# Performance work log

Measured on AMD Instinct MI355X. Metric: run time of the kernel, lower is better.

Reference implementation:

```python
import jax, jax.numpy as jnp
import numpy as np

DIM = 192
R = 16            # patches_resolution, D=H=W=R
SP = 4            # split_size
NH = 6            # num_heads (block level); per-branch heads = NH//3
B = 2
L = R * R * R
EPS = 1e-5


def layernorm(x, g, b):
    mu = jnp.mean(x, axis=-1, keepdims=True)
    var = jnp.mean(jnp.square(x - mu), axis=-1, keepdims=True)
    return (x - mu) * jax.lax.rsqrt(var + EPS) * g + b


def window_partition(x, d_sp, h_sp, w_sp, nh):
    b, _, _, _, cb = x.shape
    win = d_sp * h_sp * w_sp
    x = x.reshape(b, R // d_sp, d_sp, R // h_sp, h_sp, R // w_sp, w_sp, cb)
    x = x.transpose(0, 1, 3, 5, 2, 4, 6, 7).reshape(-1, win, nh, cb // nh)
    return x.transpose(0, 2, 1, 3)


def window_merge(x, d_sp, h_sp, w_sp, b):
    cb = x.shape[-1]
    x = x.reshape(b, R // d_sp, R // h_sp, R // w_sp, d_sp, h_sp, w_sp, cb)
    x = x.transpose(0, 1, 4, 2, 5, 3, 6, 7).reshape(b, L, cb)
    return x


def lepe_attention(q, k, v, d_sp, h_sp, w_sp, nh):
    # q,k,v: (B, L, Cb). Note: LePE bias is computed-but-unused in the source -> pure windowed SDPA.
    b, _, cb = q.shape
    hd = cb // nh
    scale = hd ** -0.5
    q5 = q.reshape(b, R, R, R, cb)
    k5 = k.reshape(b, R, R, R, cb)
    v5 = v.reshape(b, R, R, R, cb)
    qw = window_partition(q5, d_sp, h_sp, w_sp, nh) * scale
    kw = window_partition(k5, d_sp, h_sp, w_sp, nh)
    vw = window_partition(v5, d_sp, h_sp, w_sp, nh)
    attn = jax.nn.softmax(jnp.einsum('whqd,whkd->whqk', qw, kw), axis=-1)
    out = jnp.einsum('whqk,whkd->whqd', attn, vw)
    out = out.transpose(0, 2, 1, 3).reshape(-1, d_sp * h_sp * w_sp, cb)
    return window_merge(out, d_sp, h_sp, w_sp, b)


WINDOW_SHAPES = [(R, R, SP), (R, SP, R), (SP, R, R)]  # idx 0,1,2


def setup_inputs() -> dict:
    key = jax.random.key(0)
    ks = jax.random.split(key, 12)
    C = DIM
    H4 = int(C * 4)
    inp = {
        'x': jax.random.normal(ks[0], (B, C, R, R, R), dtype=jnp.float32),
        'w_qkv': jax.random.normal(ks[1], (C, 3 * C), dtype=jnp.float32) * (C ** -0.5),
        'w_proj': jax.random.normal(ks[2], (C, C), dtype=jnp.float32) * (C ** -0.5),
        'b_proj': jnp.zeros((C,), dtype=jnp.float32),
        'g1': jnp.ones((C,), dtype=jnp.float32),
        'b1': jnp.zeros((C,), dtype=jnp.float32),
        'g2': jnp.ones((C,), dtype=jnp.float32),
        'b2': jnp.zeros((C,), dtype=jnp.float32),
        'w_fc1': jax.random.normal(ks[3], (C, H4), dtype=jnp.float32) * (C ** -0.5),
        'b_fc1': jnp.zeros((H4,), dtype=jnp.float32),
        'w_fc2': jax.random.normal(ks[4], (H4, C), dtype=jnp.float32) * (H4 ** -0.5),
        'b_fc2': jnp.zeros((C,), dtype=jnp.float32),
    }
    return inp


def reference(x, w_qkv, w_proj, b_proj, g1, b1, g2, b2, w_fc1, b_fc1, w_fc2, b_fc2):
    C = DIM
    Cb = C // 3
    nh_b = NH // 3
    x = 2.0 * x
    xt = jnp.transpose(x, (0, 2, 3, 4, 1))                # (B, D, H, W, C)
    img = layernorm(xt, g1, b1)
    qkv = img.reshape(B, L, C) @ w_qkv                    # (B, L, 3C)
    q, k, v = jnp.split(qkv.reshape(B, L, 3, C).transpose(2, 0, 1, 3), 3, axis=0)
    q, k, v = q[0], k[0], v[0]                            # each (B, L, C)
    outs = []
    for i, (dsp, hsp, wsp) in enumerate(WINDOW_SHAPES):
        sl = slice(i * Cb, (i + 1) * Cb)
        outs.append(lepe_attention(q[..., sl], k[..., sl], v[..., sl], dsp, hsp, wsp, nh_b))
    attened = jnp.concatenate(outs, axis=2)               # (B, L, C)
    attened = attened @ w_proj + b_proj
    xs = xt.reshape(B, L, C) + attened
    h = layernorm(xs, g2, b2) @ w_fc1 + b_fc1
    h = jax.nn.gelu(h, approximate=False)
    xs = xs + (h @ w_fc2 + b_fc2)
    out = xs.reshape(B, R, R, R, C).transpose(0, 4, 1, 2, 3)  # (B, C, D, H, W)
    return out
```

## Files before the change

### kernel.cpp

```cpp
#include <hip/hip_runtime.h>
#include <hip/hip_bf16.h>

typedef __hip_bfloat16 bf16;
typedef short short8 __attribute__((ext_vector_type(8)));
typedef float floatx4 __attribute__((ext_vector_type(4)));

#define SZ (8192*192)

__device__ __forceinline__ unsigned short f2b(float f) {
    unsigned u = __builtin_bit_cast(unsigned, f);
    u += 0x7FFFu + ((u >> 16) & 1u);
    return (unsigned short)(u >> 16);
}
__device__ __forceinline__ float b2f(unsigned short h) {
    unsigned u = ((unsigned)h) << 16;
    return __builtin_bit_cast(float, u);
}
__device__ __forceinline__ unsigned pk2(float a, float b) {
    return ((unsigned)f2b(b) << 16) | (unsigned)f2b(a);
}

__global__ void detect_kernel(const unsigned short* __restrict__ x16, int* __restrict__ flag) {
    __shared__ int cnt;
    if (threadIdx.x == 0) cnt = 0;
    __syncthreads();
    int c = 0;
    for (int i = threadIdx.x; i < 8192; i += 256) {
        int e = (x16[i] >> 7) & 0xFF;
        if (e >= 152) c++;
    }
    if (c) atomicAdd(&cnt, c);
    __syncthreads();
    if (threadIdx.x == 0) *flag = (cnt >= 32) ? 1 : 0;
}

struct WPA { const void* s[11]; };

__global__ __launch_bounds__(256) void wprep_kernel(WPA a, unsigned short* __restrict__ wdst,
                                                    float* __restrict__ vdst,
                                                    const int* __restrict__ flag) {
    int i = blockIdx.x * 256 + threadIdx.x;
    int f = *flag;
    if (i < 442368) {
        int seg, base, K, N;
        if (i < 110592)      { seg = 0; base = 0;      K = 192; N = 576; }
        else if (i < 147456) { seg = 1; base = 110592; K = 192; N = 192; }
        else if (i < 294912) { seg = 2; base = 147456; K = 192; N = 768; }
        else                 { seg = 3; base = 294912; K = 768; N = 192; }
        int j = i - base;
        int n = j / K, k = j - n * K;
        size_t src = (size_t)k * N + n;
        float v = f ? ((const float*)a.s[seg])[src] : b2f(((const unsigned short*)a.s[seg])[src]);
        wdst[i] = f2b(v);
    } else if (i < 444288) {
        int j = i - 442368;
        int seg, off;
        if (j < 960)       { seg = 4 + j / 192; off = j % 192; }
        else if (j < 1728) { seg = 9; off = j - 960; }
        else               { seg = 10; off = j - 1728; }
        float v = f ? ((const float*)a.s[seg])[off] : b2f(((const unsigned short*)a.s[seg])[off]);
        vdst[j] = v;
    }
}

__global__ __launch_bounds__(256) void prep_kernel(const void* __restrict__ xin,
        const int* __restrict__ flag,
        const float* __restrict__ g1, const float* __restrict__ b1,
        float* __restrict__ xt, unsigned short* __restrict__ img) {
    __shared__ float tile[192][33];
    __shared__ float mu[32], rs[32];
    int tid = threadIdx.x;
    int t0 = blockIdx.x * 32;
    int b = t0 >> 12;
    int ts = t0 & 4095;
    int f = *flag;
    for (int idx = tid; idx < 192 * 32; idx += 256) {
        int c = idx >> 5, tt = idx & 31;
        int gi = ((b * 192 + c) << 12) + ts + tt;
        float raw = f ? ((const float*)xin)[gi] : b2f(((const unsigned short*)xin)[gi]);
        tile[c][tt] = 2.0f * raw;
    }
    __syncthreads();
    if (tid < 32) {
        float s = 0.f, sq = 0.f;
        for (int c = 0; c < 192; ++c) { float v = tile[c][tid]; s += v; sq += v * v; }
        float m = s * (1.0f / 192.0f);
        float var = sq * (1.0f / 192.0f) - m * m;
        mu[tid] = m;
        rs[tid] = rsqrtf(var + 1e-5f);
    }
    __syncthreads();
    for (int idx = tid; idx < 32 * 192; idx += 256) {
        int tt = idx / 192, c = idx % 192;
        float v = tile[c][tt];
        int o = (t0 + tt) * 192 + c;
        xt[o] = v;
        img[o] = f2b((v - mu[tt]) * rs[tt] * g1[c] + b1[c]);
    }
}

template <int MODE>
__global__ __launch_bounds__(256) void mfma_gemm(const unsigned short* __restrict__ A,
        const unsigned short* __restrict__ WT, const float* __restrict__ bias,
        const float* __restrict__ resid, void* __restrict__ out, int M, int N, int K) {
    int wave = threadIdx.x >> 6, lane = threadIdx.x & 63;
    int quad = lane >> 4, l16 = lane & 15;
    int m0 = blockIdx.x * 128, n0 = blockIdx.y * 64;
    const unsigned short* ap = A + (size_t)(m0 + wave * 32 + l16) * K + quad * 8;
    const unsigned short* wp = WT + (size_t)(n0 + l16) * K + quad * 8;
    floatx4 acc[2][4] = {};
    #pragma unroll 2
    for (int kc = 0; kc < K; kc += 32) {
        short8 a0 = *reinterpret_cast<const short8*>(ap + kc);
        short8 a1 = *reinterpret_cast<const short8*>(ap + (size_t)16 * K + kc);
        #pragma unroll
        for (int nt = 0; nt < 4; ++nt) {
            short8 w = *reinterpret_cast<const short8*>(wp + (size_t)nt * 16 * K + kc);
            acc[0][nt] = __builtin_amdgcn_mfma_f32_16x16x32_bf16(a0, w, acc[0][nt], 0, 0, 0);
            acc[1][nt] = __builtin_amdgcn_mfma_f32_16x16x32_bf16(a1, w, acc[1][nt], 0, 0, 0);
        }
    }
    #pragma unroll
    for (int fh = 0; fh < 2; ++fh) {
        #pragma unroll
        for (int nt = 0; nt < 4; ++nt) {
            #pragma unroll
            for (int r = 0; r < 4; ++r) {
                int row = m0 + wave * 32 + fh * 16 + quad * 4 + r;
                int col = n0 + nt * 16 + l16;
                float v = acc[fh][nt][r];
                if (MODE == 0 && col < 192) v *= 0.17677669529663689f;
                if (MODE >= 1) v += bias[col];
                if (MODE == 2) v = 0.5f * v * (1.0f + erff(v * 0.70710678118654752f));
                size_t o = (size_t)row * N + col;
                if (MODE == 0 || MODE == 2) ((unsigned short*)out)[o] = f2b(v);
                else                        ((float*)out)[o] = v + resid[o];
            }
        }
    }
}

__device__ __forceinline__ int tok_of(int br, int wb, int q) {
    if (br == 0) return ((q >> 6) << 8) | (((q >> 2) & 15) << 4) | (wb << 2) | (q & 3);
    else if (br == 1) return ((q >> 6) << 8) | (((wb << 2) + ((q >> 4) & 3)) << 4) | (q & 15);
    else return (((wb << 2) + (q >> 8)) << 8) | (q & 255);
}

__device__ __forceinline__ int vtaddr(int d) { return d * 72 + ((d >> 3) << 3); }

__device__ __forceinline__ const short8* kvptr(const unsigned short* __restrict__ qkv,
                                               int tb, int br, int wb, int q, int off) {
    int t = tok_of(br, wb, q);
    return reinterpret_cast<const short8*>(qkv + (size_t)(tb + t) * 576 + off);
}

template <int SPLIT>
__global__ __launch_bounds__(256) void attn_mfma(const unsigned short* __restrict__ qkv,
        unsigned short* __restrict__ attb, float* __restrict__ po, float* __restrict__ pl) {
    __shared__ __align__(16) unsigned short P[4][16 * 72];
    __shared__ __align__(16) unsigned short VT[2][32 * 72 + 32];
    const int chunk = 96 * SPLIT;
    int hw = blockIdx.x;
    int bid = (hw & 7) * chunk + (hw >> 3);
    int kh, rest;
    if (SPLIT == 2) { kh = bid & 1; rest = bid >> 1; }
    else            { kh = 0;       rest = bid; }
    int qt = rest & 15, head = (rest >> 4) & 1, wb = (rest >> 5) & 3, b = (rest >> 7) & 1, br = rest >> 8;
    int tid = threadIdx.x;
    int wave = tid >> 6, lane = tid & 63, quad = lane >> 4, l16 = lane & 15;
    int coff = br * 64 + head * 32;
    int tb = b << 12;
    int tq = tok_of(br, wb, qt * 64 + wave * 16 + l16);
    short8 aq = *reinterpret_cast<const short8*>(qkv + (size_t)(tb + tq) * 576 + coff + quad * 8);
    floatx4 o0 = {}, o1 = {};
    float lsum[4] = {0.f, 0.f, 0.f, 0.f};
    unsigned short* Pw = P[wave];
    int vkey5 = lane >> 2;
    int vd = lane & 3;
    int vcol = 4 * vkey5 + wave;

    const int NT = 16 / SPLIT;
    const int kt0 = kh * NT;

    short8 vv, k0, k1, k2, k3;
    {
        int kc = kt0 * 64;
        vv = *kvptr(qkv, tb, br, wb, kc + wave * 16 + vkey5, 384 + coff + vd * 8);
        k0 = *kvptr(qkv, tb, br, wb, kc + l16,      192 + coff + quad * 8);
        k1 = *kvptr(qkv, tb, br, wb, kc + 16 + l16, 192 + coff + quad * 8);
        k2 = *kvptr(qkv, tb, br, wb, kc + 32 + l16, 192 + coff + quad * 8);
        k3 = *kvptr(qkv, tb, br, wb, kc + 48 + l16, 192 + coff + quad * 8);
    }

    for (int it = 0; it < NT; ++it) {
        unsigned short* VTb = VT[it & 1];
        #pragma unroll
        for (int j = 0; j < 8; ++j)
            VTb[vtaddr(vd * 8 + j) + vcol] = (unsigned short)vv[j];
        short8 ck0 = k0, ck1 = k1, ck2 = k2, ck3 = k3;
        if (it + 1 < NT) {
            int kc = (kt0 + it + 1) * 64;
            vv = *kvptr(qkv, tb, br, wb, kc + wave * 16 + vkey5, 384 + coff + vd * 8);
            k0 = *kvptr(qkv, tb, br, wb, kc + l16,      192 + coff + quad * 8);
            k1 = *kvptr(qkv, tb, br, wb, kc + 16 + l16, 192 + coff + quad * 8);
            k2 = *kvptr(qkv, tb, br, wb, kc + 32 + l16, 192 + coff + quad * 8);
            k3 = *kvptr(qkv, tb, br, wb, kc + 48 + l16, 192 + coff + quad * 8);
        }
        __syncthreads();
        floatx4 z = {};
        floatx4 s0 = __builtin_amdgcn_mfma_f32_16x16x32_bf16(aq, ck0, z, 0, 0, 0);
        floatx4 s1 = __builtin_amdgcn_mfma_f32_16x16x32_bf16(aq, ck1, z, 0, 0, 0);
        floatx4 s2 = __builtin_amdgcn_mfma_f32_16x16x32_bf16(aq, ck2, z, 0, 0, 0);
        floatx4 s3 = __builtin_amdgcn_mfma_f32_16x16x32_bf16(aq, ck3, z, 0, 0, 0);
        #pragma unroll
        for (int r = 0; r < 4; ++r) {
            float p0 = __expf(s0[r]);
            float p1 = __expf(s1[r]);
            float p2 = __expf(s2[r]);
            float p3 = __expf(s3[r]);
            lsum[r] += (p0 + p1) + (p2 + p3);
            uint2 w2; w2.x = pk2(p0, p1); w2.y = pk2(p2, p3);
            *reinterpret_cast<uint2*>(Pw + (quad * 4 + r) * 72 + 4 * l16) = w2;
        }
        const unsigned short* pr = Pw + l16 * 72;
        short8 a0 = *reinterpret_cast<const short8*>(pr + quad * 8);
        short8 a1 = *reinterpret_cast<const short8*>(pr + 32 + quad * 8);
        const unsigned short* v0r = VTb + vtaddr(l16);
        const unsigned short* v1r = VTb + vtaddr(16 + l16);
        short8 b00 = *reinterpret_cast<const short8*>(v0r + quad * 8);
        short8 b01 = *reinterpret_cast<const short8*>(v0r + 32 + quad * 8);
        short8 b10 = *reinterpret_cast<const short8*>(v1r + quad * 8);
        short8 b11 = *reinterpret_cast<const short8*>(v1r + 32 + quad * 8);
        o0 = __builtin_amdgcn_mfma_f32_16x16x32_bf16(a0, b00, o0, 0, 0, 0);
        o0 = __builtin_amdgcn_mfma_f32_16x16x32_bf16(a1, b01, o0, 0, 0, 0);
        o1 = __builtin_amdgcn_mfma_f32_16x16x32_bf16(a0, b10, o1, 0, 0, 0);
        o1 = __builtin_amdgcn_mfma_f32_16x16x32_bf16(a1, b11, o1, 0, 0, 0);
    }
    #pragma unroll
    for (int r = 0; r < 4; ++r) {
        float ls = lsum[r];
        ls += __shfl_xor(ls, 1);
        ls += __shfl_xor(ls, 2);
        ls += __shfl_xor(ls, 4);
        ls += __shfl_xor(ls, 8);
        lsum[r] = ls;
    }
    if (SPLIT == 2) {
        #pragma unroll
        for (int r = 0; r < 4; ++r) {
            int q = qt * 64 + wave * 16 + quad * 4 + r;
            int t = tok_of(br, wb, q);
            size_t o = ((size_t)(kh << 13) + tb + t) * 192 + coff;
            po[o + l16]      = o0[r];
            po[o + 16 + l16] = o1[r];
            if (l16 == 0) pl[(size_t)((kh << 13) + tb + t) * 6 + br * 2 + head] = lsum[r];
        }
    } else {
        #pragma unroll
        for (int r = 0; r < 4; ++r) {
            float inv = 1.0f / lsum[r];
            int q = qt * 64 + wave * 16 + quad * 4 + r;
            int t = tok_of(br, wb, q);
            size_t o = (size_t)(tb + t) * 192 + coff;
            attb[o + l16]      = f2b(o0[r] * inv);
            attb[o + 16 + l16] = f2b(o1[r] * inv);
        }
    }
}

__global__ __launch_bounds__(256) void attn_combine(const float* __restrict__ po,
        const float* __restrict__ pl, unsigned short* __restrict__ attb) {
    int token = (blockIdx.x << 2) + (threadIdx.x >> 6);
    int lane = threadIdx.x & 63;
    const float* r0 = po + (size_t)token * 192;
    const float* r1 = r0 + (size_t)8192 * 192;
    const float* q0 = pl + (size_t)token * 6;
    const float* q1 = q0 + (size_t)8192 * 6;
    unsigned short* orow = attb + (size_t)token * 192;
    #pragma unroll
    for (int sgm = 0; sgm < 3; ++sgm) {
        int d = lane + sgm * 64;
        int g = d >> 5;
        float denom = q0[g] + q1[g];
        orow[d] = f2b((r0[d] + r1[d]) / denom);
    }
}

__global__ __launch_bounds__(256) void ln_kernel(const float* __restrict__ in,
        const float* __restrict__ g, const float* __restrict__ bb, unsigned short* __restrict__ out) {
    int token = (blockIdx.x << 2) + (threadIdx.x >> 6);
    int lane = threadIdx.x & 63;
    const float* row = in + (size_t)token * 192;
    float v0 = row[lane], v1 = row[lane + 64], v2 = row[lane + 128];
    float s = v0 + v1 + v2, sq = v0 * v0 + v1 * v1 + v2 * v2;
    #pragma unroll
    for (int mask = 1; mask < 64; mask <<= 1) {
        s += __shfl_xor(s, mask);
        sq += __shfl_xor(sq, mask);
    }
    float m = s * (1.f / 192.f);
    float var = sq * (1.f / 192.f) - m * m;
    float rsd = rsqrtf(var + 1e-5f);
    unsigned short* orow = out + (size_t)token * 192;
    orow[lane]       = f2b((v0 - m) * rsd * g[lane]       + bb[lane]);
    orow[lane + 64]  = f2b((v1 - m) * rsd * g[lane + 64]  + bb[lane + 64]);
    orow[lane + 128] = f2b((v2 - m) * rsd * g[lane + 128] + bb[lane + 128]);
}

__global__ __launch_bounds__(256) void unprep_kernel(const float* __restrict__ xs,
                                                     void* __restrict__ out,
                                                     const int* __restrict__ flag) {
    __shared__ float tile[192][33];
    int tid = threadIdx.x;
    int t0 = blockIdx.x * 32;
    int b = t0 >> 12, ts = t0 & 4095;
    for (int idx = tid; idx < 32 * 192; idx += 256) {
        int tt = idx / 192, c = idx % 192;
        tile[c][tt] = xs[(size_t)(t0 + tt) * 192 + c];
    }
    __syncthreads();
    int f = *flag;
    for (int idx = tid; idx < 192 * 32; idx += 256) {
        int c = idx >> 5, tt = idx & 31;
        float v = tile[c][tt];
        int o = ((b * 192 + c) << 12) + ts + tt;
        if (f) ((float*)out)[o] = v;
        else   ((unsigned short*)out)[o] = f2b(v);
    }
}

extern "C" void kernel_launch(void* const* d_in, const int* in_sizes, int n_in,
                              void* d_out, int out_size, void* d_ws, size_t ws_size,
                              hipStream_t stream) {
    float* ws = (float*)d_ws;

    float* vbase = ws;
    float* bprojf = vbase + 0;
    float* g1f    = vbase + 192;
    float* b1f    = vbase + 384;
    float* g2f    = vbase + 576;
    float* b2f    = vbase + 768;
    float* bfc1f  = vbase + 960;
    float* bfc2f  = vbase + 1728;

    unsigned short* wbase = (unsigned short*)(ws + 1920);
    unsigned short* wqkvT = wbase + 0;
    unsigned short* wprojT = wbase + 110592;
    unsigned short* wfc1T = wbase + 147456;
    unsigned short* wfc2T = wbase + 294912;

    size_t p = 1920 + 442368 / 2;
    float* xt = ws + p; p += SZ;
    unsigned short* img = (unsigned short*)(ws + p); p += SZ / 2;
    size_t pQ = p;
    unsigned short* qkv = (unsigned short*)(ws + pQ);
    unsigned short* hbuf = (unsigned short*)(ws + pQ);
    p = pQ + 8192 * 768 / 2;
    unsigned short* attb = (unsigned short*)(ws + p); p += SZ / 2;
    int* flag = (int*)(ws + p); p += 16;
    float* po = ws + p; p += (size_t)2 * 8192 * 192;
    float* pl = ws + p; p += (size_t)2 * 8192 * 6;
    bool split_ok = ws_size >= p * sizeof(float);
    float* xs = xt;
    unsigned short* lnb = img;

    WPA wa;
    wa.s[0] = d_in[1];  wa.s[1] = d_in[2];  wa.s[2] = d_in[8];  wa.s[3] = d_in[10];
    wa.s[4] = d_in[3];  wa.s[5] = d_in[4];  wa.s[6] = d_in[5];  wa.s[7] = d_in[6];
    wa.s[8] = d_in[7];  wa.s[9] = d_in[9];  wa.s[10] = d_in[11];

    detect_kernel<<<dim3(1), dim3(256), 0, stream>>>((const unsigned short*)d_in[0], flag);
    wprep_kernel<<<dim3(1736), dim3(256), 0, stream>>>(wa, wbase, vbase, flag);
    prep_kernel<<<dim3(256), dim3(256), 0, stream>>>(d_in[0], flag, g1f, b1f, xt, img);
    mfma_gemm<0><<<dim3(64, 9), dim3(256), 0, stream>>>(img, wqkvT, nullptr, nullptr, qkv, 8192, 576, 192);
    if (split_ok) {
        attn_mfma<2><<<dim3(1536), dim3(256), 0, stream>>>(qkv, nullptr, po, pl);
        attn_combine<<<dim3(2048), dim3(256), 0, stream>>>(po, pl, attb);
    } else {
        attn_mfma<1><<<dim3(768), dim3(256), 0, stream>>>(qkv, attb, nullptr, nullptr);
    }
    mfma_gemm<1><<<dim3(64, 3), dim3(256), 0, stream>>>(attb, wprojT, bprojf, xt, xs, 8192, 192, 192);
    ln_kernel<<<dim3(2048), dim3(256), 0, stream>>>(xs, g2f, b2f, lnb);
    mfma_gemm<2><<<dim3(64, 12), dim3(256), 0, stream>>>(lnb, wfc1T, bfc1f, nullptr, hbuf, 8192, 768, 192);
    mfma_gemm<3><<<dim3(64, 3), dim3(256), 0, stream>>>(hbuf, wfc2T, bfc2f, xs, xs, 8192, 192, 768);
    unprep_kernel<<<dim3(256), dim3(256), 0, stream>>>(xs, d_out, flag);
}
```

Baseline: 211.9 us.

## Fuse attention combine into proj GEMM and output transpose into FC2 epilogue

Removes the attn_combine kernel by having the projection GEMM read the two fp32 partial attention outputs and log-sum denominators, normalising and converting them to bf16 on the fly as its A operand. Removes unprep_kernel by writing the FC2 result, plus residual, directly in channel-major output layout inside the GEMM epilogue. It also halves the GEMM M tile to 64 rows to launch twice as many blocks. In exchange, the proj GEMM does uncoalesced scalar fp32 loads in its inner loop, and the FC2 epilogue makes strided transposed stores without staging through LDS.

```diff
diff --git a/kernel.cpp b/kernel.cpp
--- a/kernel.cpp
+++ b/kernel.cpp
@@ -99,42 +99,74 @@
     }
 }
 
-template <int MODE>
+template <int MODE, int TM>
 __global__ __launch_bounds__(256) void mfma_gemm(const unsigned short* __restrict__ A,
+        const float* __restrict__ pA, const float* __restrict__ pl,
         const unsigned short* __restrict__ WT, const float* __restrict__ bias,
-        const float* __restrict__ resid, void* __restrict__ out, int M, int N, int K) {
+        const float* __restrict__ resid, void* __restrict__ out,
+        const int* __restrict__ flag, int N, int K) {
     int wave = threadIdx.x >> 6, lane = threadIdx.x & 63;
     int quad = lane >> 4, l16 = lane & 15;
-    int m0 = blockIdx.x * 128, n0 = blockIdx.y * 64;
-    const unsigned short* ap = A + (size_t)(m0 + wave * 32 + l16) * K + quad * 8;
+    int m0 = blockIdx.x * TM, n0 = blockIdx.y * 64;
+    constexpr int FH = TM / 64;
+    int arow = m0 + wave * (TM / 4) + l16;
+    const unsigned short* ap = A + (size_t)arow * K + quad * 8;
     const unsigned short* wp = WT + (size_t)(n0 + l16) * K + quad * 8;
-    floatx4 acc[2][4] = {};
+    floatx4 acc[FH][4] = {};
+    float inv6[6];
+    const float* prow0 = nullptr;
+    if constexpr (MODE == 4) {
+        prow0 = pA + (size_t)arow * 192;
+        #pragma unroll
+        for (int g = 0; g < 6; ++g)
+            inv6[g] = 1.0f / (pl[(size_t)arow * 6 + g] + pl[(size_t)(8192 + arow) * 6 + g]);
+    }
     #pragma unroll 2
     for (int kc = 0; kc < K; kc += 32) {
-        short8 a0 = *reinterpret_cast<const short8*>(ap + kc);
-        short8 a1 = *reinterpret_cast<const short8*>(ap + (size_t)16 * K + kc);
+        short8 a0, a1;
+        if constexpr (MODE == 4) {
+            float iv = inv6[kc >> 5];
+            const float* p0 = prow0 + kc + quad * 8;
+            const float* p1 = p0 + (size_t)8192 * 192;
+            #pragma unroll
+            for (int j = 0; j < 8; ++j) a0[j] = (short)f2b((p0[j] + p1[j]) * iv);
+        } else {
+            a0 = *reinterpret_cast<const short8*>(ap + kc);
+            if constexpr (FH == 2) a1 = *reinterpret_cast<const short8*>(ap + (size_t)16 * K + kc);
+        }
         #pragma unroll
         for (int nt = 0; nt < 4; ++nt) {
             short8 w = *reinterpret_cast<const short8*>(wp + (size_t)nt * 16 * K + kc);
             acc[0][nt] = __builtin_amdgcn_mfma_f32_16x16x32_bf16(a0, w, acc[0][nt], 0, 0, 0);
-            acc[1][nt] = __builtin_amdgcn_mfma_f32_16x16x32_bf16(a1, w, acc[1][nt], 0, 0, 0);
-        }
-    }
+            if constexpr (FH == 2)
+                acc[1][nt] = __builtin_amdgcn_mfma_f32_16x16x32_bf16(a1, w, acc[1][nt], 0, 0, 0);
+        }
+    }
+    int f = 0;
+    if constexpr (MODE == 5) f = *flag;
     #pragma unroll
-    for (int fh = 0; fh < 2; ++fh) {
+    for (int fh = 0; fh < FH; ++fh) {
         #pragma unroll
         for (int nt = 0; nt < 4; ++nt) {
             #pragma unroll
             for (int r = 0; r < 4; ++r) {
-                int row = m0 + wave * 32 + fh * 16 + quad * 4 + r;
+                int row = m0 + wave * (TM / 4) + fh * 16 + quad * 4 + r;
                 int col = n0 + nt * 16 + l16;
                 float v = acc[fh][nt][r];
                 if (MODE == 0 && col < 192) v *= 0.17677669529663689f;
                 if (MODE >= 1) v += bias[col];
                 if (MODE == 2) v = 0.5f * v * (1.0f + erff(v * 0.70710678118654752f));
-                size_t o = (size_t)row * N + col;
-                if (MODE == 0 || MODE == 2) ((unsigned short*)out)[o] = f2b(v);
-                else                        ((float*)out)[o] = v + resid[o];
+                if constexpr (MODE == 5) {
+                    v += resid[(size_t)row * 192 + col];
+                    int bb_ = row >> 12, t = row & 4095;
+                    size_t o = ((size_t)(bb_ * 192 + col) << 12) + t;
+                    if (f) ((float*)out)[o] = v;
+                    else   ((unsigned short*)out)[o] = f2b(v);
+                } else {
+                    size_t o = (size_t)row * N + col;
+                    if (MODE == 0 || MODE == 2) ((unsigned short*)out)[o] = f2b(v);
+                    else                        ((float*)out)[o] = v + resid[o];
+                }
             }
         }
     }
@@ -268,24 +300,6 @@
     }
 }
 
-__global__ __launch_bounds__(256) void attn_combine(const float* __restrict__ po,
-        const float* __restrict__ pl, unsigned short* __restrict__ attb) {
-    int token = (blockIdx.x << 2) + (threadIdx.x >> 6);
-    int lane = threadIdx.x & 63;
-    const float* r0 = po + (size_t)token * 192;
-    const float* r1 = r0 + (size_t)8192 * 192;
-    const float* q0 = pl + (size_t)token * 6;
-    const float* q1 = q0 + (size_t)8192 * 6;
-    unsigned short* orow = attb + (size_t)token * 192;
-    #pragma unroll
-    for (int sgm = 0; sgm < 3; ++sgm) {
-        int d = lane + sgm * 64;
-        int g = d >> 5;
-        float denom = q0[g] + q1[g];
-        orow[d] = f2b((r0[d] + r1[d]) / denom);
-    }
-}
-
 __global__ __launch_bounds__(256) void ln_kernel(const float* __restrict__ in,
         const float* __restrict__ g, const float* __restrict__ bb, unsigned short* __restrict__ out) {
     int token = (blockIdx.x << 2) + (threadIdx.x >> 6);
@@ -305,28 +319,6 @@
     orow[lane]       = f2b((v0 - m) * rsd * g[lane]       + bb[lane]);
     orow[lane + 64]  = f2b((v1 - m) * rsd * g[lane + 64]  + bb[lane + 64]);
     orow[lane + 128] = f2b((v2 - m) * rsd * g[lane + 128] + bb[lane + 128]);
-}
-
-__global__ __launch_bounds__(256) void unprep_kernel(const float* __restrict__ xs,
-                                                     void* __restrict__ out,
-                                                     const int* __restrict__ flag) {
-    __shared__ float tile[192][33];
-    int tid = threadIdx.x;
-    int t0 = blockIdx.x * 32;
-    int b = t0 >> 12, ts = t0 & 4095;
-    for (int idx = tid; idx < 32 * 192; idx += 256) {
-        int tt = idx / 192, c = idx % 192;
-        tile[c][tt] = xs[(size_t)(t0 + tt) * 192 + c];
-    }
-    __syncthreads();
-    int f = *flag;
-    for (int idx = tid; idx < 192 * 32; idx += 256) {
-        int c = idx >> 5, tt = idx & 31;
-        float v = tile[c][tt];
-        int o = ((b * 192 + c) << 12) + ts + tt;
-        if (f) ((float*)out)[o] = v;
-        else   ((unsigned short*)out)[o] = f2b(v);
-    }
 }
 
 extern "C" void kernel_launch(void* const* d_in, const int* in_sizes, int n_in,
@@ -372,16 +364,20 @@
     detect_kernel<<<dim3(1), dim3(256), 0, stream>>>((const unsigned short*)d_in[0], flag);
     wprep_kernel<<<dim3(1736), dim3(256), 0, stream>>>(wa, wbase, vbase, flag);
     prep_kernel<<<dim3(256), dim3(256), 0, stream>>>(d_in[0], flag, g1f, b1f, xt, img);
-    mfma_gemm<0><<<dim3(64, 9), dim3(256), 0, stream>>>(img, wqkvT, nullptr, nullptr, qkv, 8192, 576, 192);
+    mfma_gemm<0, 64><<<dim3(128, 9), dim3(256), 0, stream>>>(
+        img, nullptr, nullptr, wqkvT, nullptr, nullptr, qkv, nullptr, 576, 192);
     if (split_ok) {
         attn_mfma<2><<<dim3(1536), dim3(256), 0, stream>>>(qkv, nullptr, po, pl);
-        attn_combine<<<dim3(2048), dim3(256), 0, stream>>>(po, pl, attb);
+        mfma_gemm<4, 64><<<dim3(128, 3), dim3(256), 0, stream>>>(
+            (const unsigned short*)po, po, pl, wprojT, bprojf, xt, xs, nullptr, 192, 192);
     } else {
         attn_mfma<1><<<dim3(768), dim3(256), 0, stream>>>(qkv, attb, nullptr, nullptr);
-    }
-    mfma_gemm<1><<<dim3(64, 3), dim3(256), 0, stream>>>(attb, wprojT, bprojf, xt, xs, 8192, 192, 192);
+        mfma_gemm<1, 64><<<dim3(128, 3), dim3(256), 0, stream>>>(
+            attb, nullptr, nullptr, wprojT, bprojf, xt, xs, nullptr, 192, 192);
+    }
     ln_kernel<<<dim3(2048), dim3(256), 0, stream>>>(xs, g2f, b2f, lnb);
-    mfma_gemm<2><<<dim3(64, 12), dim3(256), 0, stream>>>(lnb, wfc1T, bfc1f, nullptr, hbuf, 8192, 768, 192);
-    mfma_gemm<3><<<dim3(64, 3), dim3(256), 0, stream>>>(hbuf, wfc2T, bfc2f, xs, xs, 8192, 192, 768);
-    unprep_kernel<<<dim3(256), dim3(256), 0, stream>>>(xs, d_out, flag);
-}
+    mfma_gemm<2, 64><<<dim3(128, 12), dim3(256), 0, stream>>>(
+        lnb, nullptr, nullptr, wfc1T, bfc1f, nullptr, hbuf, nullptr, 768, 192);
+    mfma_gemm<5, 64><<<dim3(128, 3), dim3(256), 0, stream>>>(
+        hbuf, nullptr, nullptr, wfc2T, bfc2f, xs, d_out, flag, 192, 768);
+}
```

New measurement: 235.3 us. 11.0% more time.
